# Kernel tuning notes

Hardware: AMD Instinct MI355X
Metric: run time of the kernel (lower is better)

The kernel has to match this reference:

```python
import jax, jax.numpy as jnp
import numpy as np

N = 16384   # total nodes in batch
E = 65536   # edges
B = 512     # sessions
L = 32      # nodes per session
H = 64      # hidden_size
HEADS = 16  # GAT heads (layer 1)
K = 3       # interests
V = 32000   # n_node (item vocab)
NEG = 0.2   # leaky relu slope


def _u(k, shape, stdv):
    return jax.random.uniform(k, shape, jnp.float32, -stdv, stdv)


def setup_inputs():
    key = jax.random.key(0)
    ks = jax.random.split(key, 24)
    s = 1.0 / np.sqrt(H)  # reset_parameters: uniform(-stdv, stdv)
    D = K * H
    return {
        "x": jax.random.randint(ks[0], (N,), 0, V),
        "edge_index": jax.random.randint(ks[1], (2, E), 0, N),
        "batch": jnp.repeat(jnp.arange(B, dtype=jnp.int32), L),
        "embedding": _u(ks[2], (V, H), s),
        "w_interest": _u(ks[3], (H, K), s),
        "gat1_W": _u(ks[4], (K, H, HEADS * H), s),
        "gat1_as": _u(ks[5], (K, HEADS, H), s),
        "gat1_ad": _u(ks[6], (K, HEADS, H), s),
        "gat1_b": _u(ks[7], (K, HEADS * H), s),
        "gat2_W": _u(ks[8], (K, HEADS * H, H), s),
        "gat2_as": _u(ks[9], (K, 1, H), s),
        "gat2_ad": _u(ks[10], (K, 1, H), s),
        "gat2_b": _u(ks[11], (K, H), s),
        "W1_w": _u(ks[12], (D, D), s), "W1_b": _u(ks[13], (D,), s),
        "W2_w": _u(ks[14], (D, D), s), "W2_b": _u(ks[15], (D,), s),
        "q_w": _u(ks[16], (D, 1), s), "q_b": _u(ks[17], (1,), s),
        "W3_w": _u(ks[18], (2 * D, D), s), "W3_b": _u(ks[19], (D,), s),
    }


def _gat(h_in, W, b, a_s, a_d, src, dst, valid, heads, out):
    """PyG GATConv: per-head linear, edge softmax over dest, self-loops for all nodes."""
    n = h_in.shape[0]
    h = (h_in @ W).reshape(n, heads, out)          # [n, heads, out]
    asrc = (h * a_s[None]).sum(-1)                 # [n, heads]
    adst = (h * a_d[None]).sum(-1)
    loop = jnp.arange(n)
    fs = jnp.concatenate([src, loop])              # edges + self-loops
    fd = jnp.concatenate([dst, loop])
    v = jnp.concatenate([valid, jnp.ones((n,), bool)])
    logits = jax.nn.leaky_relu(asrc[fs] + adst[fd], NEG)   # [E+n, heads]
    logits = jnp.where(v[:, None], logits, -1e9)
    m = jax.ops.segment_max(logits, fd, num_segments=n)
    p = jnp.exp(logits - m[fd]) * v[:, None]
    denom = jax.ops.segment_sum(p, fd, num_segments=n)     # [n, heads]
    num = jax.ops.segment_sum(p[:, :, None] * h[fs], fd, num_segments=n)
    return (num / denom[:, :, None]).reshape(n, heads * out) + b


def _model(x, edge_index, batch, embedding, w_interest,
           gat1_W, gat1_as, gat1_ad, gat1_b,
           gat2_W, gat2_as, gat2_ad, gat2_b,
           W1_w, W1_b, W2_w, W2_b, q_w, q_b, W3_w, W3_b):
    e = embedding[x]                                # [N, H]
    g = jax.nn.softmax((e @ w_interest) / 0.1, axis=-1)   # [N, K]
    mask = g > (1.0 / K)                            # interest_mask
    src, dst = edge_index[0], edge_index[1]
    hiddens = []
    for i in range(K):                              # fixed small interest loop
        xi = g[:, i:i + 1] * e                      # einsum('ik,il->ikl')[:, i]
        valid = mask[src, i] & mask[dst, i]         # subgraph edge mask
        h1 = jax.nn.relu(_gat(xi, gat1_W[i], gat1_b[i], gat1_as[i], gat1_ad[i],
                              src, dst, valid, HEADS, H))
        h2 = _gat(h1, gat2_W[i], gat2_b[i], gat2_as[i], gat2_ad[i],
                  src, dst, valid, 1, H)
        hiddens.append(h2)
    sess = jnp.concatenate(hiddens, axis=1)         # [N, K*H]
    # Embedding2Score
    last_idx = jax.ops.segment_max(jnp.arange(N), batch, num_segments=B)
    v_n = sess[last_idx]                            # [B, K*H]  last node per session
    q1 = v_n[batch] @ W1_w + W1_b                   # v_n repeated per node
    q2 = sess @ W2_w + W2_b
    alpha = jax.nn.sigmoid(q1 + q2) @ q_w + q_b     # [N, 1]
    s_g = jax.ops.segment_sum(alpha * sess, batch, num_segments=B)
    s_h = jnp.concatenate([v_n, s_g], axis=1) @ W3_w + W3_b   # [B, K*H]
    s_h = s_h.reshape(B * K, H)                     # multi-interest split
    z = s_h @ embedding.T                           # [B*K, V]
    return z.reshape(B, K, V).max(axis=1)           # [B, V]


def reference(x, edge_index, batch, embedding, w_interest,
              gat1_W, gat1_as, gat1_ad, gat1_b,
              gat2_W, gat2_as, gat2_ad, gat2_b,
              W1_w, W1_b, W2_w, W2_b, q_w, q_b, W3_w, W3_b):
    return _model(x, edge_index, batch, embedding, w_interest,
                  gat1_W, gat1_as, gat1_ad, gat1_b,
                  gat2_W, gat2_as, gat2_ad, gat2_b,
                  W1_w, W1_b, W2_w, W2_b, q_w, q_b, W3_w, W3_b)
```

## Files before the change

kernel.cpp:

```cpp
#include <hip/hip_runtime.h>
#include <math.h>

#define NN 16384
#define EE 65536
#define BB 512
#define VV 32000

typedef unsigned short us_t;
typedef unsigned int u32_t;
typedef __attribute__((ext_vector_type(4))) float f32x4;
typedef __attribute__((ext_vector_type(8))) short bf16x8;

__device__ __forceinline__ float bf2f(unsigned int u) {
  return __uint_as_float((u & 0xffffu) << 16);
}
__device__ __forceinline__ unsigned short f2bf(float f) {
  unsigned int x = __float_as_uint(f);
  unsigned int r = (x + 0x7fffu + ((x >> 16) & 1u)) >> 16;
  return (unsigned short)r;
}
__device__ __forceinline__ float wsum(float v) {
#pragma unroll
  for (int o = 32; o; o >>= 1) v += __shfl_xor(v, o, 64);
  return v;
}
__device__ __forceinline__ float redu16(float v) {
  v += __shfl_xor(v, 1, 64);
  v += __shfl_xor(v, 2, 64);
  v += __shfl_xor(v, 4, 64);
  v += __shfl_xor(v, 8, 64);
  return v;
}
__device__ __forceinline__ float lrelu(float x) { return x > 0.f ? x : 0.2f * x; }

__global__ void k_detect(const void* emb, int* flag) {
  if (threadIdx.x == 0 && blockIdx.x == 0) {
    const us_t* u = (const us_t*)emb;
    int ok = 1;
    for (int i = 0; i < 128; i++) {
      float v = bf2f((unsigned int)u[i]);
      if (!(fabsf(v) <= 0.13f)) { ok = 0; break; }
    }
    *flag = ok;
  }
}

struct PrepArgs {
  const void* src[17];
  void* dst[17];
  int n[17];
  int kind[17];
  int start[18];
};

__global__ void k_prep(PrepArgs pa, const int* __restrict__ flag) {
  int blk = blockIdx.x;
  int s = 0;
  while (s < 16 && blk >= pa.start[s + 1]) s++;
  int i = (blk - pa.start[s]) * 256 + threadIdx.x;
  if (i >= pa.n[s]) return;
  float v = (*flag) ? bf2f((unsigned int)((const us_t*)pa.src[s])[i])
                    : ((const float*)pa.src[s])[i];
  int kind = pa.kind[s];
  if (kind == 0) {
    ((float*)pa.dst[s])[i] = v;
  } else if (kind == 1) {
    ((us_t*)pa.dst[s])[i] = f2bf(v);
  } else if (kind == 2) {
    int ii = i >> 16, r = i & 65535, k = r >> 10, col = r & 1023;
    ((us_t*)pa.dst[s])[(ii << 16) + col * 64 + k] = f2bf(v);
  } else if (kind == 3) {
    int ii = i >> 16, r = i & 65535, k = r >> 6, col = r & 63;
    ((us_t*)pa.dst[s])[(ii << 16) + col * 1024 + k] = f2bf(v);
  } else {
    int k = i / 192, col = i % 192;
    ((us_t*)pa.dst[s])[col * 192 + k] = f2bf(v);
  }
}

__global__ void k_prepWa(const void* __restrict__ g1Wraw,
                         const float* __restrict__ g1as, const float* __restrict__ g1ad,
                         const int* __restrict__ flag, us_t* __restrict__ Waspack) {
  int gid = blockIdx.x * 256 + threadIdx.x;
  if (gid >= 96 * 64) return;
  int c = gid >> 6, k = gid & 63;
  int i = c >> 5, sd = (c >> 4) & 1, h = c & 15;
  const float* av = (sd ? g1ad : g1as) + i * 1024 + h * 64;
  size_t base = (size_t)i * 65536 + (size_t)k * 1024 + h * 64;
  int isbf = *flag;
  float s = 0.f;
  for (int d = 0; d < 64; d++) {
    float wv = isbf ? bf2f((unsigned int)((const us_t*)g1Wraw)[base + d])
                    : ((const float*)g1Wraw)[base + d];
    s += wv * av[d];
  }
  Waspack[c * 64 + k] = f2bf(s);
}

__global__ void k_embed(const int* __restrict__ x, const void* __restrict__ embr,
                        const void* __restrict__ wintr, const int* __restrict__ flag,
                        us_t* __restrict__ e_bf, float* __restrict__ g) {
  int gid = blockIdx.x * blockDim.x + threadIdx.x;
  int n = gid >> 6, lane = gid & 63;
  if (n >= NN) return;
  int isbf = *flag;
  size_t ei = (size_t)x[n] * 64 + lane;
  float v = isbf ? bf2f((unsigned int)((const us_t*)embr)[ei]) : ((const float*)embr)[ei];
  e_bf[(size_t)n * 64 + lane] = f2bf(v);
  float w0, w1, w2;
  if (isbf) {
    const us_t* w = (const us_t*)wintr;
    w0 = bf2f(w[lane * 3 + 0]); w1 = bf2f(w[lane * 3 + 1]); w2 = bf2f(w[lane * 3 + 2]);
  } else {
    const float* w = (const float*)wintr;
    w0 = w[lane * 3 + 0]; w1 = w[lane * 3 + 1]; w2 = w[lane * 3 + 2];
  }
  float t0 = wsum(v * w0), t1 = wsum(v * w1), t2 = wsum(v * w2);
  if (lane == 0) {
    float l0 = t0 / 0.1f, l1 = t1 / 0.1f, l2 = t2 / 0.1f;
    float m = fmaxf(l0, fmaxf(l1, l2));
    float p0 = __expf(l0 - m), p1 = __expf(l1 - m), p2 = __expf(l2 - m);
    float inv = 1.0f / (p0 + p1 + p2);
    g[n * 4 + 0] = p0 * inv; g[n * 4 + 1] = p1 * inv;
    g[n * 4 + 2] = p2 * inv; g[n * 4 + 3] = 0.f;
  }
}

__global__ void k_countv(const int* __restrict__ ei, const float* __restrict__ g,
                         int* __restrict__ countsv) {
  int e = blockIdx.x * 256 + threadIdx.x;
  if (e >= EE) return;
  int s = ei[e], d = ei[EE + e];
  const float thr = 1.0f / 3.0f;
#pragma unroll
  for (int i = 0; i < 3; i++) {
    if (g[s * 4 + i] > thr && g[d * 4 + i] > thr)
      atomicAdd(&countsv[i * NN + d], 1);
  }
}

__global__ void k_scanv(const int* __restrict__ counts, int* __restrict__ offsets) {
  __shared__ int part[256];
  __shared__ int excl[257];
  int t = threadIdx.x;
  int base = t * 192;
  int s = 0;
  for (int j = 0; j < 192; j++) s += counts[base + j];
  part[t] = s;
  __syncthreads();
  if (t == 0) {
    int run = 0;
    for (int j = 0; j < 256; j++) { excl[j] = run; run += part[j]; }
    excl[256] = run;
  }
  __syncthreads();
  int run = excl[t];
  for (int j = 0; j < 192; j++) { offsets[base + j] = run; run += counts[base + j]; }
  if (t == 255) offsets[3 * NN] = excl[256];
}

__global__ void k_fillv(const int* __restrict__ ei, const float* __restrict__ g,
                        const float* __restrict__ eatt,
                        const int* __restrict__ offsetsv, int* __restrict__ fillposv,
                        int2* __restrict__ edgesC, float* __restrict__ easrcP) {
  int e = blockIdx.x * 256 + threadIdx.x;
  if (e >= EE) return;
  int s = ei[e], d = ei[EE + e];
  const float thr = 1.0f / 3.0f;
#pragma unroll
  for (int i = 0; i < 3; i++) {
    float gs = g[s * 4 + i];
    if (gs > thr && g[d * 4 + i] > thr) {
      int pos = offsetsv[i * NN + d] + atomicAdd(&fillposv[i * NN + d], 1);
      edgesC[pos] = make_int2(s, __float_as_int(gs));
      const float* er = &eatt[(size_t)s * 96 + i * 32];
      float* op = &easrcP[(size_t)pos * 16];
#pragma unroll
      for (int h = 0; h < 16; h++) op[h] = gs * er[h];
    }
  }
}

__global__ __launch_bounds__(256) void k_easrc(
    const us_t* __restrict__ e_bf, const us_t* __restrict__ Waspack,
    float* __restrict__ eatt) {
  __shared__ char As[8192];
  int t = threadIdx.x;
  int row0 = blockIdx.x * 64;
  for (int id = t; id < 512; id += 256) {
    int r = id >> 3, c = id & 7;
    uint4 v = *(const uint4*)&e_bf[(size_t)(row0 + r) * 64 + c * 8];
    *(uint4*)(As + r * 128 + ((c ^ (r & 7)) << 4)) = v;
  }
  __syncthreads();
  int wv = t >> 6, L = t & 63, li = L & 15, lq = L >> 4;
#pragma unroll
  for (int ct = 0; ct < 6; ct++) {
    f32x4 acc = {0.f, 0.f, 0.f, 0.f};
#pragma unroll
    for (int ks = 0; ks < 2; ks++) {
      int row = wv * 16 + li;
      bf16x8 af = *(const bf16x8*)(As + row * 128 + (((ks * 4 + lq) ^ (row & 7)) << 4));
      bf16x8 bfr = *(const bf16x8*)(Waspack + (size_t)(ct * 16 + li) * 64 + ks * 32 + lq * 8);
      acc = __builtin_amdgcn_mfma_f32_16x16x32_bf16(af, bfr, acc, 0, 0, 0);
    }
#pragma unroll
    for (int r = 0; r < 4; r++) {
      int row = row0 + wv * 16 + lq * 4 + r;
      eatt[(size_t)row * 96 + ct * 16 + li] = acc[r];
    }
  }
}

__global__ __launch_bounds__(256) void k_phaseA(
    const us_t* __restrict__ e_bf, const float* __restrict__ g,
    const float* __restrict__ eatt,
    const int* __restrict__ offsetsv, const int2* __restrict__ edgesC,
    const float* __restrict__ easrcP, us_t* __restrict__ xagg) {
  int t = threadIdx.x;
  int intr = blockIdx.y;
  int wv = t >> 6, L = t & 63;
  int n = blockIdx.x * 4 + wv;
  int h = L >> 2;
  int doff = (L & 3) * 16;
  float gn = g[n * 4 + intr];
  float ad = gn * eatt[(size_t)n * 96 + intr * 32 + 16 + h];
  float m = lrelu(gn * eatt[(size_t)n * 96 + intr * 32 + h] + ad);
  float den = 1.f;
  float acc[16];
  {
    const uint4* ep = (const uint4*)&e_bf[(size_t)n * 64 + doff];
    uint4 a = ep[0], b = ep[1];
    acc[0] = gn * bf2f(a.x);  acc[1] = gn * bf2f(a.x >> 16);
    acc[2] = gn * bf2f(a.y);  acc[3] = gn * bf2f(a.y >> 16);
    acc[4] = gn * bf2f(a.z);  acc[5] = gn * bf2f(a.z >> 16);
    acc[6] = gn * bf2f(a.w);  acc[7] = gn * bf2f(a.w >> 16);
    acc[8] = gn * bf2f(b.x);  acc[9] = gn * bf2f(b.x >> 16);
    acc[10] = gn * bf2f(b.y); acc[11] = gn * bf2f(b.y >> 16);
    acc[12] = gn * bf2f(b.z); acc[13] = gn * bf2f(b.z >> 16);
    acc[14] = gn * bf2f(b.w); acc[15] = gn * bf2f(b.w >> 16);
  }
  int beg = offsetsv[intr * NN + n], end = offsetsv[intr * NN + n + 1];
  for (int j = beg; j < end; j++) {
    int2 sg = edgesC[j];
    int s = sg.x;
    float gs = __int_as_float(sg.y);
    float l = lrelu(easrcP[(size_t)j * 16 + h] + ad);
    float p = __expf(l - m);
    den += p;
    float pg = p * gs;
    const uint4* ep = (const uint4*)&e_bf[(size_t)s * 64 + doff];
    uint4 a = ep[0], b = ep[1];
    acc[0] += pg * bf2f(a.x);  acc[1] += pg * bf2f(a.x >> 16);
    acc[2] += pg * bf2f(a.y);  acc[3] += pg * bf2f(a.y >> 16);
    acc[4] += pg * bf2f(a.z);  acc[5] += pg * bf2f(a.z >> 16);
    acc[6] += pg * bf2f(a.w);  acc[7] += pg * bf2f(a.w >> 16);
    acc[8] += pg * bf2f(b.x);  acc[9] += pg * bf2f(b.x >> 16);
    acc[10] += pg * bf2f(b.y); acc[11] += pg * bf2f(b.y >> 16);
    acc[12] += pg * bf2f(b.z); acc[13] += pg * bf2f(b.z >> 16);
    acc[14] += pg * bf2f(b.w); acc[15] += pg * bf2f(b.w >> 16);
  }
  float inv = 1.f / den;
  u32_t w[8];
#pragma unroll
  for (int kk = 0; kk < 8; kk++) {
    w[kk] = (u32_t)f2bf(acc[2 * kk] * inv) | ((u32_t)f2bf(acc[2 * kk + 1] * inv) << 16);
  }
  us_t* op = &xagg[((size_t)intr * NN + n) * 1024 + h * 64 + doff];
  *(uint4*)op = make_uint4(w[0], w[1], w[2], w[3]);
  *(uint4*)(op + 8) = make_uint4(w[4], w[5], w[6], w[7]);
}

__global__ __launch_bounds__(128) void k_phaseB(
    const us_t* __restrict__ xagg, const us_t* __restrict__ g1Wt,
    const us_t* __restrict__ g2Wt, const float* __restrict__ b1all,
    const float* __restrict__ g2as, const float* __restrict__ g2ad,
    us_t* __restrict__ h2pre, float* __restrict__ a2s, float* __restrict__ a2d) {
  __shared__ char Tb[2][2][4096];
  __shared__ float b1s[1024];
  __shared__ float a2v[128];
  int t = threadIdx.x;
  int wv = t >> 6, L = t & 63, li = L & 15, lq = L >> 4;
  int intr = blockIdx.y;
  int n0 = blockIdx.x * 64 + wv * 32;
  const us_t* Wt1 = g1Wt + (size_t)intr * 65536;
  const us_t* Wt2 = g2Wt + (size_t)intr * 65536;
  const us_t* xa = xagg + ((size_t)intr * NN + n0 - (size_t)wv * 32 + (size_t)wv * 32) * 1024;
  for (int id = t; id < 1024; id += 128) b1s[id] = b1all[intr * 1024 + id];
  if (t < 64) a2v[t] = g2as[intr * 64 + t];
  else a2v[t] = g2ad[intr * 64 + (t - 64)];
  __syncthreads();
  f32x4 acc2[4][2];
#pragma unroll
  for (int ca = 0; ca < 4; ca++)
#pragma unroll
    for (int nb = 0; nb < 2; nb++) acc2[ca][nb] = {0.f, 0.f, 0.f, 0.f};
  for (int hh = 0; hh < 16; hh++) {
    bf16x8 bx[2][2];
#pragma unroll
    for (int nb = 0; nb < 2; nb++)
#pragma unroll
      for (int ks = 0; ks < 2; ks++)
        bx[nb][ks] = *(const bf16x8*)&xa[(size_t)(nb * 16 + li) * 1024 + hh * 64 + ks * 32 + lq * 8];
    f32x4 c1[4][2];
#pragma unroll
    for (int ct = 0; ct < 4; ct++)
#pragma unroll
      for (int nb = 0; nb < 2; nb++) c1[ct][nb] = {0.f, 0.f, 0.f, 0.f};
#pragma unroll
    for (int ks = 0; ks < 2; ks++) {
#pragma unroll
      for (int ct = 0; ct < 4; ct++) {
        bf16x8 af = *(const bf16x8*)&Wt1[(size_t)(hh * 64 + ct * 16 + li) * 64 + ks * 32 + lq * 8];
#pragma unroll
        for (int nb = 0; nb < 2; nb++)
          c1[ct][nb] = __builtin_amdgcn_mfma_f32_16x16x32_bf16(af, bx[nb][ks], c1[ct][nb], 0, 0, 0);
      }
    }
    char* Th = &Tb[wv][hh & 1][0];
#pragma unroll
    for (int ct = 0; ct < 4; ct++) {
      float b0 = b1s[hh * 64 + ct * 16 + lq * 4 + 0];
      float b1v = b1s[hh * 64 + ct * 16 + lq * 4 + 1];
      float b2 = b1s[hh * 64 + ct * 16 + lq * 4 + 2];
      float b3 = b1s[hh * 64 + ct * 16 + lq * 4 + 3];
#pragma unroll
      for (int nb = 0; nb < 2; nb++) {
        int node = nb * 16 + li;
        u32_t p0 = (u32_t)f2bf(fmaxf(c1[ct][nb][0] + b0, 0.f)) |
                   ((u32_t)f2bf(fmaxf(c1[ct][nb][1] + b1v, 0.f)) << 16);
        u32_t p1 = (u32_t)f2bf(fmaxf(c1[ct][nb][2] + b2, 0.f)) |
                   ((u32_t)f2bf(fmaxf(c1[ct][nb][3] + b3, 0.f)) << 16);
        int ch = (ct * 2 + (lq >> 1)) ^ (node & 7);
        *(uint2*)(Th + node * 128 + (ch << 4) + ((lq & 1) * 8)) = make_uint2(p0, p1);
      }
    }
#pragma unroll
    for (int ks2 = 0; ks2 < 2; ks2++) {
      bf16x8 bt[2];
#pragma unroll
      for (int nb = 0; nb < 2; nb++) {
        int node = nb * 16 + li;
        int ch = (ks2 * 4 + lq) ^ (node & 7);
        bt[nb] = *(const bf16x8*)(Th + node * 128 + (ch << 4));
      }
#pragma unroll
      for (int ca = 0; ca < 4; ca++) {
        bf16x8 af2 = *(const bf16x8*)&Wt2[(size_t)(ca * 16 + li) * 1024 + hh * 64 + ks2 * 32 + lq * 8];
#pragma unroll
        for (int nb = 0; nb < 2; nb++)
          acc2[ca][nb] = __builtin_amdgcn_mfma_f32_16x16x32_bf16(af2, bt[nb], acc2[ca][nb], 0, 0, 0);
      }
    }
  }
  float asv[16], adv[16];
#pragma unroll
  for (int ca = 0; ca < 4; ca++)
#pragma unroll
    for (int r = 0; r < 4; r++) {
      asv[ca * 4 + r] = a2v[ca * 16 + lq * 4 + r];
      adv[ca * 4 + r] = a2v[64 + ca * 16 + lq * 4 + r];
    }
#pragma unroll
  for (int nb = 0; nb < 2; nb++) {
    float ps = 0.f, pd = 0.f;
#pragma unroll
    for (int ca = 0; ca < 4; ca++)
#pragma unroll
      for (int r = 0; r < 4; r++) {
        float v = acc2[ca][nb][r];
        ps += v * asv[ca * 4 + r];
        pd += v * adv[ca * 4 + r];
      }
    ps += __shfl_xor(ps, 16, 64); ps += __shfl_xor(ps, 32, 64);
    pd += __shfl_xor(pd, 16, 64); pd += __shfl_xor(pd, 32, 64);
    if (lq == 0) {
      a2s[(size_t)intr * NN + n0 + nb * 16 + li] = ps;
      a2d[(size_t)intr * NN + n0 + nb * 16 + li] = pd;
    }
  }
  char* Tr = &Tb[wv][0][0];
#pragma unroll
  for (int ca = 0; ca < 4; ca++)
#pragma unroll
    for (int nb = 0; nb < 2; nb++) {
      int node = nb * 16 + li;
      u32_t p0 = (u32_t)f2bf(acc2[ca][nb][0]) | ((u32_t)f2bf(acc2[ca][nb][1]) << 16);
      u32_t p1 = (u32_t)f2bf(acc2[ca][nb][2]) | ((u32_t)f2bf(acc2[ca][nb][3]) << 16);
      int ch = (ca * 2 + (lq >> 1)) ^ (node & 7);
      *(uint2*)(Tr + node * 128 + (ch << 4) + ((lq & 1) * 8)) = make_uint2(p0, p1);
    }
  asm volatile("s_waitcnt lgkmcnt(0)" ::: "memory");
  {
    int row = L >> 1, hc = (L & 1) * 4;
#pragma unroll
    for (int cc = 0; cc < 4; cc++) {
      int ch = (hc + cc) ^ (row & 7);
      uint4 v = *(const uint4*)(Tr + row * 128 + (ch << 4));
      *(uint4*)&h2pre[((size_t)intr * NN + n0 + row) * 64 + (hc + cc) * 8] = v;
    }
  }
}

__global__ void k_gat2_agg(const us_t* __restrict__ h2pre_a,
                           const float* __restrict__ a2s_a, const float* __restrict__ a2d_a,
                           const float* __restrict__ b2all,
                           const int* __restrict__ offsetsv,
                           const int2* __restrict__ edgesC, float* __restrict__ sess) {
  int intr = blockIdx.y;
  int gid = blockIdx.x * blockDim.x + threadIdx.x;
  int n = gid >> 6, lane = gid & 63;
  if (n >= NN) return;
  const us_t* h2pre = h2pre_a + (size_t)intr * NN * 64;
  const float* a2s = a2s_a + (size_t)intr * NN;
  const float* a2d = a2d_a + (size_t)intr * NN;
  const float* b2 = b2all + intr * 64;
  float ad = a2d[n];
  float m = lrelu(a2s[n] + ad);
  float den = 1.f;
  float acc = bf2f((unsigned int)h2pre[(size_t)n * 64 + lane]);
  int beg = offsetsv[intr * NN + n], end = offsetsv[intr * NN + n + 1];
  for (int j = beg; j < end; j++) {
    int s = edgesC[j].x;
    float l = lrelu(a2s[s] + ad);
    float p = __expf(l - m);
    den += p;
    acc += p * bf2f((unsigned int)h2pre[(size_t)s * 64 + lane]);
  }
  sess[(size_t)n * 192 + intr * 64 + lane] = acc / den + b2[lane];
}

__global__ __launch_bounds__(192) void k_vq1(
    const float* __restrict__ sess,
    const float* __restrict__ W1w, const float* __restrict__ W1b,
    float* __restrict__ vn, float* __restrict__ vq1) {
  __shared__ float row[192];
  int b = blockIdx.x, j = threadIdx.x;
  int li = b * 32 + 31;
  float v = sess[(size_t)li * 192 + j];
  row[j] = v;
  vn[b * 192 + j] = v;
  __syncthreads();
  float acc = W1b[j];
  for (int k = 0; k < 192; k++) acc += row[k] * W1w[k * 192 + j];
  vq1[b * 192 + j] = acc;
}

__global__ __launch_bounds__(256) void k_alpha_sg_mfma(
    const float* __restrict__ sess, const float* __restrict__ vq1,
    const us_t* __restrict__ W2T, const float* __restrict__ W2b,
    const float* __restrict__ qw, const float* __restrict__ qb,
    float* __restrict__ sg) {
  __shared__ char As[64 * 512];
  __shared__ float vq_l[2 * 192];
  __shared__ float w2b_l[192], qw_l[192];
  __shared__ float sg_l[2 * 192];
  int t = threadIdx.x;
  int n0 = blockIdx.x * 64;
  if (t < 192) { w2b_l[t] = W2b[t]; qw_l[t] = qw[t]; }
  for (int id = t; id < 384; id += 256) {
    sg_l[id] = 0.f;
    vq_l[id] = vq1[(size_t)(blockIdx.x * 2) * 192 + id];
  }
  for (int id = t; id < 1536; id += 256) {
    int r = id / 24, c = id % 24;
    const float* p = &sess[(size_t)(n0 + r) * 192 + c * 8];
    float4 f0 = *(const float4*)p;
    float4 f1 = *(const float4*)(p + 4);
    u32_t w0 = (u32_t)f2bf(f0.x) | ((u32_t)f2bf(f0.y) << 16);
    u32_t w1 = (u32_t)f2bf(f0.z) | ((u32_t)f2bf(f0.w) << 16);
    u32_t w2 = (u32_t)f2bf(f1.x) | ((u32_t)f2bf(f1.y) << 16);
    u32_t w3 = (u32_t)f2bf(f1.z) | ((u32_t)f2bf(f1.w) << 16);
    *(uint4*)(As + r * 512 + ((c ^ (r & 7)) << 4)) = make_uint4(w0, w1, w2, w3);
  }
  __syncthreads();
  int wv = t >> 6, lane = t & 63, li = lane & 15, lq = lane >> 4;
  int sl = wv >> 1;
  f32x4 acc[12];
#pragma unroll
  for (int sub = 0; sub < 12; sub++) acc[sub] = {0.f, 0.f, 0.f, 0.f};
#pragma unroll
  for (int ks = 0; ks < 6; ks++) {
    int r = wv * 16 + li;
    bf16x8 af = *(const bf16x8*)(As + r * 512 + (((ks * 4 + lq) ^ (r & 7)) << 4));
#pragma unroll
    for (int sub = 0; sub < 12; sub++) {
      bf16x8 bfr = *(const bf16x8*)&W2T[(size_t)(sub * 16 + li) * 192 + ks * 32 + lq * 8];
      acc[sub] = __builtin_amdgcn_mfma_f32_16x16x32_bf16(af, bfr, acc[sub], 0, 0, 0);
    }
  }
  float qbv = qb[0];
  float s_part[12];
#pragma unroll
  for (int sub = 0; sub < 12; sub++) s_part[sub] = 0.f;
#pragma unroll
  for (int rr = 0; rr < 4; rr++) {
    int n = n0 + wv * 16 + lq * 4 + rr;
    float ap = 0.f;
    float sv[12];
#pragma unroll
    for (int sub = 0; sub < 12; sub++) {
      int col = sub * 16 + li;
      float q = vq_l[sl * 192 + col] + acc[sub][rr] + w2b_l[col];
      float sgm = 1.f / (1.f + __expf(-q));
      ap += sgm * qw_l[col];
      sv[sub] = sess[(size_t)n * 192 + col];
    }
    ap = redu16(ap);
    float alpha = ap + qbv;
#pragma unroll
    for (int sub = 0; sub < 12; sub++) s_part[sub] += alpha * sv[sub];
  }
#pragma unroll
  for (int sub = 0; sub < 12; sub++) {
    float v = s_part[sub];
    v += __shfl_xor(v, 16, 64);
    v += __shfl_xor(v, 32, 64);
    if (lq == 0) atomicAdd(&sg_l[sl * 192 + sub * 16 + li], v);
  }
  __syncthreads();
  for (int id = t; id < 384; id += 256)
    sg[(size_t)(blockIdx.x * 2) * 192 + id] = sg_l[id];
}

__global__ __launch_bounds__(192) void k_sh(
    const float* __restrict__ vn, const float* __restrict__ sg,
    const float* __restrict__ W3w, const float* __restrict__ W3b,
    float* __restrict__ sh) {
  __shared__ float row[384];
  int b = blockIdx.x, j = threadIdx.x;
  row[j] = vn[b * 192 + j];
  row[192 + j] = sg[b * 192 + j];
  __syncthreads();
  float acc = W3b[j];
  for (int k = 0; k < 384; k++) acc += row[k] * W3w[k * 192 + j];
  sh[b * 192 + j] = acc;
}

__global__ __launch_bounds__(256) void k_final_mfma(
    const float* __restrict__ sh, const us_t* __restrict__ emb_bf,
    void* __restrict__ out, const int* __restrict__ flag) {
  __shared__ uint4 AsU[384];
  __shared__ uint4 BsU[2048];
  char* As = (char*)AsU;
  char* Bs = (char*)BsU;
  int t = threadIdx.x;
  int v0 = blockIdx.x * 256, b0 = blockIdx.y * 16;
  for (int id = t; id < 384; id += 256) {
    int i2 = id >> 7, rem = id & 127, r = rem >> 3, c = rem & 7;
    const float* p = &sh[(size_t)(b0 + r) * 192 + i2 * 64 + c * 8];
    float4 f0 = *(const float4*)p;
    float4 f1 = *(const float4*)(p + 4);
    u32_t w0 = (u32_t)f2bf(f0.x) | ((u32_t)f2bf(f0.y) << 16);
    u32_t w1 = (u32_t)f2bf(f0.z) | ((u32_t)f2bf(f0.w) << 16);
    u32_t w2 = (u32_t)f2bf(f1.x) | ((u32_t)f2bf(f1.y) << 16);
    u32_t w3 = (u32_t)f2bf(f1.z) | ((u32_t)f2bf(f1.w) << 16);
    *(uint4*)(As + i2 * 2048 + r * 128 + ((c ^ (r & 7)) << 4)) = make_uint4(w0, w1, w2, w3);
  }
  for (int id = t; id < 2048; id += 256) {
    int vr = id >> 3, c = id & 7;
    uint4 v = *(const uint4*)&emb_bf[(size_t)(v0 + vr) * 64 + c * 8];
    *(uint4*)(Bs + vr * 128 + ((c ^ (vr & 7)) << 4)) = v;
  }
  __syncthreads();
  int wv = t >> 6, lane = t & 63, li = lane & 15, lq = lane >> 4;
  int cb = wv * 64;
  int isbf = *flag;
  f32x4 acc[3][4];
#pragma unroll
  for (int i = 0; i < 3; i++)
#pragma unroll
    for (int sub = 0; sub < 4; sub++) acc[i][sub] = {0.f, 0.f, 0.f, 0.f};
#pragma unroll
  for (int ks = 0; ks < 2; ks++) {
    bf16x8 bfr[4];
#pragma unroll
    for (int sub = 0; sub < 4; sub++) {
      int vr = cb + sub * 16 + li;
      bfr[sub] = *(const bf16x8*)(Bs + vr * 128 + ((((ks << 2) | lq) ^ (vr & 7)) << 4));
    }
#pragma unroll
    for (int i = 0; i < 3; i++) {
      bf16x8 af = *(const bf16x8*)(As + i * 2048 + li * 128 + ((((ks << 2) | lq) ^ (li & 7)) << 4));
#pragma unroll
      for (int sub = 0; sub < 4; sub++)
        acc[i][sub] = __builtin_amdgcn_mfma_f32_16x16x32_bf16(af, bfr[sub], acc[i][sub], 0, 0, 0);
    }
  }
#pragma unroll
  for (int sub = 0; sub < 4; sub++) {
    int col = v0 + cb + sub * 16 + li;
#pragma unroll
    for (int rr = 0; rr < 4; rr++) {
      float o = fmaxf(fmaxf(acc[0][sub][rr], acc[1][sub][rr]), acc[2][sub][rr]);
      int b = b0 + lq * 4 + rr;
      if (isbf) ((us_t*)out)[(size_t)b * VV + col] = f2bf(o);
      else ((float*)out)[(size_t)b * VV + col] = o;
    }
  }
}

extern "C" void kernel_launch(void* const* d_in, const int* in_sizes, int n_in,
                              void* d_out, int out_size, void* d_ws, size_t ws_size,
                              hipStream_t stream) {
  if (n_in < 21) return;
  const int* x = (const int*)d_in[0];
  const int* ei = (const int*)d_in[1];

  char* ws = (char*)d_ws;
  size_t off = 0;
  auto A = [&](size_t bytes) -> char* {
    char* p = ws + off;
    off += (bytes + 255) & ~(size_t)255;
    return p;
  };
  int* flag = (int*)A(4);
  us_t* emb_bf = (us_t*)A((size_t)VV * 64 * 2);
  us_t* e_bf = (us_t*)A((size_t)NN * 64 * 2);
  us_t* g1Wt = (us_t*)A((size_t)3 * 65536 * 2);
  us_t* g2Wt = (us_t*)A((size_t)3 * 65536 * 2);
  us_t* W2T = (us_t*)A((size_t)36864 * 2);
  us_t* Waspack = (us_t*)A((size_t)96 * 64 * 2);
  float* eatt = (float*)A((size_t)NN * 96 * 4);
  float* c_g1as = (float*)A(3072 * 4);
  float* c_g1ad = (float*)A(3072 * 4);
  float* c_g1b = (float*)A(3072 * 4);
  float* c_g2as = (float*)A(192 * 4);
  float* c_g2ad = (float*)A(192 * 4);
  float* c_g2b = (float*)A(192 * 4);
  float* c_W1w = (float*)A(36864 * 4);
  float* c_W1b = (float*)A(192 * 4);
  float* c_W2b = (float*)A(192 * 4);
  float* c_qw = (float*)A(192 * 4);
  float* c_qb = (float*)A(4);
  float* c_W3w = (float*)A(73728 * 4);
  float* c_W3b = (float*)A(192 * 4);
  float* g_buf = (float*)A((size_t)NN * 4 * 4);
  us_t* xagg = (us_t*)A((size_t)3 * NN * 1024 * 2);
  us_t* h2pre = (us_t*)A((size_t)3 * NN * 64 * 2);
  float* a2s = (float*)A((size_t)3 * NN * 4);
  float* a2d = (float*)A((size_t)3 * NN * 4);
  float* sess = (float*)A((size_t)NN * 192 * 4);
  float* vq1 = (float*)A((size_t)BB * 192 * 4);
  float* sg = (float*)A((size_t)BB * 192 * 4);
  float* vn = (float*)A((size_t)BB * 192 * 4);
  float* shb = (float*)A((size_t)BB * 192 * 4);
  int* countsv = (int*)A((size_t)3 * NN * 4);
  int* offsetsv = (int*)A((size_t)(3 * NN + 1) * 4);
  int* fillposv = (int*)A((size_t)3 * NN * 4);
  int2* edgesC = (int2*)A((size_t)3 * EE * 8);
  float* easrcP = (float*)A((size_t)3 * EE * 16 * 4);
  if (off > ws_size) return;

  hipMemsetAsync(countsv, 0, 3 * NN * 4, stream);
  hipMemsetAsync(fillposv, 0, 3 * NN * 4, stream);

  k_detect<<<1, 64, 0, stream>>>(d_in[3], flag);

  PrepArgs pa;
  int nb = 0, idx = 0;
  auto SEC = [&](const void* s, void* d, int n, int kind) {
    pa.src[idx] = s; pa.dst[idx] = d; pa.n[idx] = n; pa.kind[idx] = kind;
    pa.start[idx] = nb; nb += (n + 255) / 256; idx++;
  };
  SEC(d_in[3], emb_bf, VV * 64, 1);
  SEC(d_in[5], g1Wt, 196608, 2);
  SEC(d_in[9], g2Wt, 196608, 3);
  SEC(d_in[15], W2T, 36864, 4);
  SEC(d_in[6], c_g1as, 3072, 0);
  SEC(d_in[7], c_g1ad, 3072, 0);
  SEC(d_in[8], c_g1b, 3072, 0);
  SEC(d_in[10], c_g2as, 192, 0);
  SEC(d_in[11], c_g2ad, 192, 0);
  SEC(d_in[12], c_g2b, 192, 0);
  SEC(d_in[13], c_W1w, 36864, 0);
  SEC(d_in[14], c_W1b, 192, 0);
  SEC(d_in[16], c_W2b, 192, 0);
  SEC(d_in[17], c_qw, 192, 0);
  SEC(d_in[18], c_qb, 1, 0);
  SEC(d_in[19], c_W3w, 73728, 0);
  SEC(d_in[20], c_W3b, 192, 0);
  pa.start[17] = nb;
  k_prep<<<nb, 256, 0, stream>>>(pa, flag);
  k_prepWa<<<24, 256, 0, stream>>>(d_in[5], c_g1as, c_g1ad, flag, Waspack);

  k_embed<<<NN * 64 / 256, 256, 0, stream>>>(x, d_in[3], d_in[4], flag, e_bf, g_buf);
  k_easrc<<<NN / 64, 256, 0, stream>>>(e_bf, Waspack, eatt);
  k_countv<<<EE / 256, 256, 0, stream>>>(ei, g_buf, countsv);
  k_scanv<<<1, 256, 0, stream>>>(countsv, offsetsv);
  k_fillv<<<EE / 256, 256, 0, stream>>>(ei, g_buf, eatt, offsetsv, fillposv,
                                        edgesC, easrcP);

  k_phaseA<<<dim3(NN / 4, 3), 256, 0, stream>>>(
      e_bf, g_buf, eatt, offsetsv, edgesC, easrcP, xagg);
  k_phaseB<<<dim3(NN / 64, 3), 128, 0, stream>>>(
      xagg, g1Wt, g2Wt, c_g1b, c_g2as, c_g2ad, h2pre, a2s, a2d);
  k_gat2_agg<<<dim3(NN * 64 / 256, 3), 256, 0, stream>>>(
      h2pre, a2s, a2d, c_g2b, offsetsv, edgesC, sess);

  k_vq1<<<BB, 192, 0, stream>>>(sess, c_W1w, c_W1b, vn, vq1);
  k_alpha_sg_mfma<<<NN / 64, 256, 0, stream>>>(sess, vq1, W2T, c_W2b, c_qw, c_qb, sg);
  k_sh<<<BB, 192, 0, stream>>>(vn, sg, c_W3w, c_W3b, shb);
  k_final_mfma<<<dim3(VV / 256, BB / 16), 256, 0, stream>>>(shb, emb_bf, d_out, flag);
}
```

Before: 280.2 us.

## Split phaseB head loop across four waves with LDS atomic reduction

Each block now covers 32 nodes with four waves, and each wave takes four of the sixteen GAT heads instead of one wave looping over all sixteen for its 32 nodes. The per-wave partial layer-2 accumulators are combined with shared-memory float atomics into a swizzled buffer, then the attention dot products and the bf16 h2pre store are done from that buffer. The xagg loads are also software-prefetched one head ahead. This raises parallelism and shortens each wave's serial dependency chain, at the cost of LDS atomics, an extra block barrier, more shared memory, and a changed summation order.

```diff
diff --git a/kernel.cpp b/kernel.cpp
--- a/kernel.cpp
+++ b/kernel.cpp
@@ -271,53 +271,64 @@
   *(uint4*)(op + 8) = make_uint4(w[4], w[5], w[6], w[7]);
 }
 
-__global__ __launch_bounds__(128) void k_phaseB(
+__global__ __launch_bounds__(256) void k_phaseB(
     const us_t* __restrict__ xagg, const us_t* __restrict__ g1Wt,
     const us_t* __restrict__ g2Wt, const float* __restrict__ b1all,
     const float* __restrict__ g2as, const float* __restrict__ g2ad,
     us_t* __restrict__ h2pre, float* __restrict__ a2s, float* __restrict__ a2d) {
-  __shared__ char Tb[2][2][4096];
+  __shared__ char Tb[4][2][4096];
+  __shared__ float h2red[32 * 64];
   __shared__ float b1s[1024];
   __shared__ float a2v[128];
   int t = threadIdx.x;
   int wv = t >> 6, L = t & 63, li = L & 15, lq = L >> 4;
   int intr = blockIdx.y;
-  int n0 = blockIdx.x * 64 + wv * 32;
+  int n0 = blockIdx.x * 32;
   const us_t* Wt1 = g1Wt + (size_t)intr * 65536;
   const us_t* Wt2 = g2Wt + (size_t)intr * 65536;
-  const us_t* xa = xagg + ((size_t)intr * NN + n0 - (size_t)wv * 32 + (size_t)wv * 32) * 1024;
-  for (int id = t; id < 1024; id += 128) b1s[id] = b1all[intr * 1024 + id];
+  const us_t* xa = xagg + ((size_t)intr * NN + n0) * 1024;
+  for (int id = t; id < 1024; id += 256) b1s[id] = b1all[intr * 1024 + id];
+  for (int id = t; id < 2048; id += 256) h2red[id] = 0.f;
   if (t < 64) a2v[t] = g2as[intr * 64 + t];
-  else a2v[t] = g2ad[intr * 64 + (t - 64)];
+  else if (t < 128) a2v[t] = g2ad[intr * 64 + (t - 64)];
   __syncthreads();
   f32x4 acc2[4][2];
 #pragma unroll
   for (int ca = 0; ca < 4; ca++)
 #pragma unroll
     for (int nb = 0; nb < 2; nb++) acc2[ca][nb] = {0.f, 0.f, 0.f, 0.f};
-  for (int hh = 0; hh < 16; hh++) {
-    bf16x8 bx[2][2];
+  int h0 = wv * 4;
+  bf16x8 bxA[2][2];
+#pragma unroll
+  for (int nb = 0; nb < 2; nb++)
+#pragma unroll
+    for (int ks = 0; ks < 2; ks++)
+      bxA[nb][ks] = *(const bf16x8*)&xa[(size_t)(nb * 16 + li) * 1024 + h0 * 64 + ks * 32 + lq * 8];
+  for (int hi = 0; hi < 4; hi++) {
+    int hh = h0 + hi;
+    int hn = h0 + ((hi + 1) & 3);
+    bf16x8 bxB[2][2];
 #pragma unroll
     for (int nb = 0; nb < 2; nb++)
 #pragma unroll
       for (int ks = 0; ks < 2; ks++)
-        bx[nb][ks] = *(const bf16x8*)&xa[(size_t)(nb * 16 + li) * 1024 + hh * 64 + ks * 32 + lq * 8];
+        bxB[nb][ks] = *(const bf16x8*)&xa[(size_t)(nb * 16 + li) * 1024 + hn * 64 + ks * 32 + lq * 8];
     f32x4 c1[4][2];
 #pragma unroll
     for (int ct = 0; ct < 4; ct++)
 #pragma unroll
       for (int nb = 0; nb < 2; nb++) c1[ct][nb] = {0.f, 0.f, 0.f, 0.f};
 #pragma unroll
-    for (int ks = 0; ks < 2; ks++) {
-#pragma unroll
-      for (int ct = 0; ct < 4; ct++) {
+    for (int ct = 0; ct < 4; ct++) {
+#pragma unroll
+      for (int ks = 0; ks < 2; ks++) {
         bf16x8 af = *(const bf16x8*)&Wt1[(size_t)(hh * 64 + ct * 16 + li) * 64 + ks * 32 + lq * 8];
 #pragma unroll
         for (int nb = 0; nb < 2; nb++)
-          c1[ct][nb] = __builtin_amdgcn_mfma_f32_16x16x32_bf16(af, bx[nb][ks], c1[ct][nb], 0, 0, 0);
+          c1[ct][nb] = __builtin_amdgcn_mfma_f32_16x16x32_bf16(af, bxA[nb][ks], c1[ct][nb], 0, 0, 0);
       }
     }
-    char* Th = &Tb[wv][hh & 1][0];
+    char* Th = &Tb[wv][hi & 1][0];
 #pragma unroll
     for (int ct = 0; ct < 4; ct++) {
       float b0 = b1s[hh * 64 + ct * 16 + lq * 4 + 0];
@@ -352,52 +363,45 @@
           acc2[ca][nb] = __builtin_amdgcn_mfma_f32_16x16x32_bf16(af2, bt[nb], acc2[ca][nb], 0, 0, 0);
       }
     }
-  }
-  float asv[16], adv[16];
-#pragma unroll
-  for (int ca = 0; ca < 4; ca++)
-#pragma unroll
-    for (int r = 0; r < 4; r++) {
-      asv[ca * 4 + r] = a2v[ca * 16 + lq * 4 + r];
-      adv[ca * 4 + r] = a2v[64 + ca * 16 + lq * 4 + r];
-    }
-#pragma unroll
-  for (int nb = 0; nb < 2; nb++) {
-    float ps = 0.f, pd = 0.f;
-#pragma unroll
-    for (int ca = 0; ca < 4; ca++)
-#pragma unroll
-      for (int r = 0; r < 4; r++) {
-        float v = acc2[ca][nb][r];
-        ps += v * asv[ca * 4 + r];
-        pd += v * adv[ca * 4 + r];
-      }
-    ps += __shfl_xor(ps, 16, 64); ps += __shfl_xor(ps, 32, 64);
-    pd += __shfl_xor(pd, 16, 64); pd += __shfl_xor(pd, 32, 64);
-    if (lq == 0) {
-      a2s[(size_t)intr * NN + n0 + nb * 16 + li] = ps;
-      a2d[(size_t)intr * NN + n0 + nb * 16 + li] = pd;
-    }
-  }
-  char* Tr = &Tb[wv][0][0];
-#pragma unroll
-  for (int ca = 0; ca < 4; ca++)
+#pragma unroll
+    for (int nb = 0; nb < 2; nb++)
+#pragma unroll
+      for (int ks = 0; ks < 2; ks++) bxA[nb][ks] = bxB[nb][ks];
+  }
+#pragma unroll
+  for (int ca = 0; ca < 4; ca++) {
 #pragma unroll
     for (int nb = 0; nb < 2; nb++) {
       int node = nb * 16 + li;
-      u32_t p0 = (u32_t)f2bf(acc2[ca][nb][0]) | ((u32_t)f2bf(acc2[ca][nb][1]) << 16);
-      u32_t p1 = (u32_t)f2bf(acc2[ca][nb][2]) | ((u32_t)f2bf(acc2[ca][nb][3]) << 16);
-      int ch = (ca * 2 + (lq >> 1)) ^ (node & 7);
-      *(uint2*)(Tr + node * 128 + (ch << 4) + ((lq & 1) * 8)) = make_uint2(p0, p1);
-    }
-  asm volatile("s_waitcnt lgkmcnt(0)" ::: "memory");
+      int sw = (node & 7) << 3;
+#pragma unroll
+      for (int r = 0; r < 4; r++) {
+        int col = ca * 16 + lq * 4 + r;
+        atomicAdd(&h2red[node * 64 + (col ^ sw)], acc2[ca][nb][r]);
+      }
+    }
+  }
+  __syncthreads();
   {
-    int row = L >> 1, hc = (L & 1) * 4;
-#pragma unroll
-    for (int cc = 0; cc < 4; cc++) {
-      int ch = (hc + cc) ^ (row & 7);
-      uint4 v = *(const uint4*)(Tr + row * 128 + (ch << 4));
-      *(uint4*)&h2pre[((size_t)intr * NN + n0 + row) * 64 + (hc + cc) * 8] = v;
+    int node = t >> 3, j0 = (t & 7) * 8;
+    int sw = (node & 7) << 3;
+    const float* hp = &h2red[node * 64 + (j0 ^ sw)];
+    float ps = 0.f, pd = 0.f;
+    u32_t pk[4];
+#pragma unroll
+    for (int jj = 0; jj < 4; jj++) {
+      float v0 = hp[2 * jj], v1 = hp[2 * jj + 1];
+      ps += v0 * a2v[j0 + 2 * jj] + v1 * a2v[j0 + 2 * jj + 1];
+      pd += v0 * a2v[64 + j0 + 2 * jj] + v1 * a2v[64 + j0 + 2 * jj + 1];
+      pk[jj] = (u32_t)f2bf(v0) | ((u32_t)f2bf(v1) << 16);
+    }
+    *(uint4*)&h2pre[((size_t)intr * NN + n0 + node) * 64 + j0] =
+        make_uint4(pk[0], pk[1], pk[2], pk[3]);
+    ps += __shfl_xor(ps, 1, 64); ps += __shfl_xor(ps, 2, 64); ps += __shfl_xor(ps, 4, 64);
+    pd += __shfl_xor(pd, 1, 64); pd += __shfl_xor(pd, 2, 64); pd += __shfl_xor(pd, 4, 64);
+    if ((t & 7) == 0) {
+      a2s[(size_t)intr * NN + n0 + node] = ps;
+      a2d[(size_t)intr * NN + n0 + node] = pd;
     }
   }
 }
@@ -693,7 +697,7 @@
 
   k_phaseA<<<dim3(NN / 4, 3), 256, 0, stream>>>(
       e_bf, g_buf, eatt, offsetsv, edgesC, easrcP, xagg);
-  k_phaseB<<<dim3(NN / 64, 3), 128, 0, stream>>>(
+  k_phaseB<<<dim3(NN / 32, 3), 256, 0, stream>>>(
       xagg, g1Wt, g2Wt, c_g1b, c_g2as, c_g2ad, h2pre, a2s, a2d);
   k_gat2_agg<<<dim3(NN * 64 / 256, 3), 256, 0, stream>>>(
       h2pre, a2s, a2d, c_g2b, offsetsv, edgesC, sess);
```

Result: slower. 320.9 us (+14.5%).

## Software-pipeline xagg loads in phaseB, process two heads per iteration, nontemporal xagg traffic

Applied to the files above, without the earlier changes.

The phaseB head loop is restructured to handle two heads per iteration and to prefetch the next pair's xagg fragments into registers while the current pair's MFMAs run. This hides global-load latency and exposes more independent MFMA chains. xagg writes in the aggregation kernel and reads in phaseB become nontemporal to avoid polluting cache with streaming data. It raises register pressure, which could lower occupancy, and the last iteration issues a wasted prefetch of heads 0-1.

```diff
diff --git a/kernel.cpp b/kernel.cpp
--- a/kernel.cpp
+++ b/kernel.cpp
@@ -10,6 +10,7 @@
 typedef unsigned int u32_t;
 typedef __attribute__((ext_vector_type(4))) float f32x4;
 typedef __attribute__((ext_vector_type(8))) short bf16x8;
+typedef __attribute__((ext_vector_type(4))) unsigned int u32x4;
 
 __device__ __forceinline__ float bf2f(unsigned int u) {
   return __uint_as_float((u & 0xffffu) << 16);
@@ -18,6 +19,13 @@
   unsigned int x = __float_as_uint(f);
   unsigned int r = (x + 0x7fffu + ((x >> 16) & 1u)) >> 16;
   return (unsigned short)r;
+}
+__device__ __forceinline__ bf16x8 ntld(const us_t* p) {
+  return __builtin_nontemporal_load((const bf16x8*)p);
+}
+__device__ __forceinline__ void ntst(us_t* p, u32_t a, u32_t b, u32_t c, u32_t d) {
+  u32x4 v = {a, b, c, d};
+  __builtin_nontemporal_store(v, (u32x4*)p);
 }
 __device__ __forceinline__ float wsum(float v) {
 #pragma unroll
@@ -267,8 +275,8 @@
     w[kk] = (u32_t)f2bf(acc[2 * kk] * inv) | ((u32_t)f2bf(acc[2 * kk + 1] * inv) << 16);
   }
   us_t* op = &xagg[((size_t)intr * NN + n) * 1024 + h * 64 + doff];
-  *(uint4*)op = make_uint4(w[0], w[1], w[2], w[3]);
-  *(uint4*)(op + 8) = make_uint4(w[4], w[5], w[6], w[7]);
+  ntst(op, w[0], w[1], w[2], w[3]);
+  ntst(op + 8, w[4], w[5], w[6], w[7]);
 }
 
 __global__ __launch_bounds__(128) void k_phaseB(
@@ -285,7 +293,7 @@
   int n0 = blockIdx.x * 64 + wv * 32;
   const us_t* Wt1 = g1Wt + (size_t)intr * 65536;
   const us_t* Wt2 = g2Wt + (size_t)intr * 65536;
-  const us_t* xa = xagg + ((size_t)intr * NN + n0 - (size_t)wv * 32 + (size_t)wv * 32) * 1024;
+  const us_t* xa = xagg + ((size_t)intr * NN + n0) * 1024;
   for (int id = t; id < 1024; id += 128) b1s[id] = b1all[intr * 1024 + id];
   if (t < 64) a2v[t] = g2as[intr * 64 + t];
   else a2v[t] = g2ad[intr * 64 + (t - 64)];
@@ -295,63 +303,98 @@
   for (int ca = 0; ca < 4; ca++)
 #pragma unroll
     for (int nb = 0; nb < 2; nb++) acc2[ca][nb] = {0.f, 0.f, 0.f, 0.f};
-  for (int hh = 0; hh < 16; hh++) {
-    bf16x8 bx[2][2];
+  bf16x8 bxa[2][2], bxb[2][2];
+#pragma unroll
+  for (int nb = 0; nb < 2; nb++)
+#pragma unroll
+    for (int ks = 0; ks < 2; ks++) {
+      bxa[nb][ks] = ntld(&xa[(size_t)(nb * 16 + li) * 1024 + ks * 32 + lq * 8]);
+      bxb[nb][ks] = ntld(&xa[(size_t)(nb * 16 + li) * 1024 + 64 + ks * 32 + lq * 8]);
+    }
+  for (int hp = 0; hp < 8; hp++) {
+    int ha = hp * 2, hb = ha + 1;
+    int hna = ((hp + 1) & 7) * 2, hnb = hna + 1;
+    bf16x8 nxa[2][2], nxb[2][2];
 #pragma unroll
     for (int nb = 0; nb < 2; nb++)
 #pragma unroll
-      for (int ks = 0; ks < 2; ks++)
-        bx[nb][ks] = *(const bf16x8*)&xa[(size_t)(nb * 16 + li) * 1024 + hh * 64 + ks * 32 + lq * 8];
-    f32x4 c1[4][2];
+      for (int ks = 0; ks < 2; ks++) {
+        nxa[nb][ks] = ntld(&xa[(size_t)(nb * 16 + li) * 1024 + hna * 64 + ks * 32 + lq * 8]);
+        nxb[nb][ks] = ntld(&xa[(size_t)(nb * 16 + li) * 1024 + hnb * 64 + ks * 32 + lq * 8]);
+      }
+    f32x4 c1a[4][2], c1b[4][2];
 #pragma unroll
     for (int ct = 0; ct < 4; ct++)
 #pragma unroll
-      for (int nb = 0; nb < 2; nb++) c1[ct][nb] = {0.f, 0.f, 0.f, 0.f};
+      for (int nb = 0; nb < 2; nb++) { c1a[ct][nb] = {0.f, 0.f, 0.f, 0.f}; c1b[ct][nb] = {0.f, 0.f, 0.f, 0.f}; }
 #pragma unroll
     for (int ks = 0; ks < 2; ks++) {
 #pragma unroll
       for (int ct = 0; ct < 4; ct++) {
-        bf16x8 af = *(const bf16x8*)&Wt1[(size_t)(hh * 64 + ct * 16 + li) * 64 + ks * 32 + lq * 8];
+        bf16x8 afa = *(const bf16x8*)&Wt1[(size_t)(ha * 64 + ct * 16 + li) * 64 + ks * 32 + lq * 8];
 #pragma unroll
         for (int nb = 0; nb < 2; nb++)
-          c1[ct][nb] = __builtin_amdgcn_mfma_f32_16x16x32_bf16(af, bx[nb][ks], c1[ct][nb], 0, 0, 0);
+          c1a[ct][nb] = __builtin_amdgcn_mfma_f32_16x16x32_bf16(afa, bxa[nb][ks], c1a[ct][nb], 0, 0, 0);
+        bf16x8 afb = *(const bf16x8*)&Wt1[(size_t)(hb * 64 + ct * 16 + li) * 64 + ks * 32 + lq * 8];
+#pragma unroll
+        for (int nb = 0; nb < 2; nb++)
+          c1b[ct][nb] = __builtin_amdgcn_mfma_f32_16x16x32_bf16(afb, bxb[nb][ks], c1b[ct][nb], 0, 0, 0);
       }
     }
-    char* Th = &Tb[wv][hh & 1][0];
+    char* Ta = &Tb[wv][0][0];
+    char* Tc = &Tb[wv][1][0];
 #pragma unroll
     for (int ct = 0; ct < 4; ct++) {
-      float b0 = b1s[hh * 64 + ct * 16 + lq * 4 + 0];
-      float b1v = b1s[hh * 64 + ct * 16 + lq * 4 + 1];
-      float b2 = b1s[hh * 64 + ct * 16 + lq * 4 + 2];
-      float b3 = b1s[hh * 64 + ct * 16 + lq * 4 + 3];
+      float ba0 = b1s[ha * 64 + ct * 16 + lq * 4 + 0];
+      float ba1 = b1s[ha * 64 + ct * 16 + lq * 4 + 1];
+      float ba2 = b1s[ha * 64 + ct * 16 + lq * 4 + 2];
+      float ba3 = b1s[ha * 64 + ct * 16 + lq * 4 + 3];
+      float bb0 = b1s[hb * 64 + ct * 16 + lq * 4 + 0];
+      float bb1 = b1s[hb * 64 + ct * 16 + lq * 4 + 1];
+      float bb2 = b1s[hb * 64 + ct * 16 + lq * 4 + 2];
+      float bb3 = b1s[hb * 64 + ct * 16 + lq * 4 + 3];
 #pragma unroll
       for (int nb = 0; nb < 2; nb++) {
         int node = nb * 16 + li;
-        u32_t p0 = (u32_t)f2bf(fmaxf(c1[ct][nb][0] + b0, 0.f)) |
-                   ((u32_t)f2bf(fmaxf(c1[ct][nb][1] + b1v, 0.f)) << 16);
-        u32_t p1 = (u32_t)f2bf(fmaxf(c1[ct][nb][2] + b2, 0.f)) |
-                   ((u32_t)f2bf(fmaxf(c1[ct][nb][3] + b3, 0.f)) << 16);
         int ch = (ct * 2 + (lq >> 1)) ^ (node & 7);
-        *(uint2*)(Th + node * 128 + (ch << 4) + ((lq & 1) * 8)) = make_uint2(p0, p1);
+        u32_t pa0 = (u32_t)f2bf(fmaxf(c1a[ct][nb][0] + ba0, 0.f)) |
+                    ((u32_t)f2bf(fmaxf(c1a[ct][nb][1] + ba1, 0.f)) << 16);
+        u32_t pa1 = (u32_t)f2bf(fmaxf(c1a[ct][nb][2] + ba2, 0.f)) |
+                    ((u32_t)f2bf(fmaxf(c1a[ct][nb][3] + ba3, 0.f)) << 16);
+        *(uint2*)(Ta + node * 128 + (ch << 4) + ((lq & 1) * 8)) = make_uint2(pa0, pa1);
+        u32_t pb0 = (u32_t)f2bf(fmaxf(c1b[ct][nb][0] + bb0, 0.f)) |
+                    ((u32_t)f2bf(fmaxf(c1b[ct][nb][1] + bb1, 0.f)) << 16);
+        u32_t pb1 = (u32_t)f2bf(fmaxf(c1b[ct][nb][2] + bb2, 0.f)) |
+                    ((u32_t)f2bf(fmaxf(c1b[ct][nb][3] + bb3, 0.f)) << 16);
+        *(uint2*)(Tc + node * 128 + (ch << 4) + ((lq & 1) * 8)) = make_uint2(pb0, pb1);
       }
     }
 #pragma unroll
     for (int ks2 = 0; ks2 < 2; ks2++) {
-      bf16x8 bt[2];
+      bf16x8 bta[2], btb[2];
 #pragma unroll
       for (int nb = 0; nb < 2; nb++) {
         int node = nb * 16 + li;
         int ch = (ks2 * 4 + lq) ^ (node & 7);
-        bt[nb] = *(const bf16x8*)(Th + node * 128 + (ch << 4));
+        bta[nb] = *(const bf16x8*)(Ta + node * 128 + (ch << 4));
+        btb[nb] = *(const bf16x8*)(Tc + node * 128 + (ch << 4));
       }
 #pragma unroll
       for (int ca = 0; ca < 4; ca++) {
-        bf16x8 af2 = *(const bf16x8*)&Wt2[(size_t)(ca * 16 + li) * 1024 + hh * 64 + ks2 * 32 + lq * 8];
+        bf16x8 af2a = *(const bf16x8*)&Wt2[(size_t)(ca * 16 + li) * 1024 + ha * 64 + ks2 * 32 + lq * 8];
 #pragma unroll
         for (int nb = 0; nb < 2; nb++)
-          acc2[ca][nb] = __builtin_amdgcn_mfma_f32_16x16x32_bf16(af2, bt[nb], acc2[ca][nb], 0, 0, 0);
+          acc2[ca][nb] = __builtin_amdgcn_mfma_f32_16x16x32_bf16(af2a, bta[nb], acc2[ca][nb], 0, 0, 0);
+        bf16x8 af2b = *(const bf16x8*)&Wt2[(size_t)(ca * 16 + li) * 1024 + hb * 64 + ks2 * 32 + lq * 8];
+#pragma unroll
+        for (int nb = 0; nb < 2; nb++)
+          acc2[ca][nb] = __builtin_amdgcn_mfma_f32_16x16x32_bf16(af2b, btb[nb], acc2[ca][nb], 0, 0, 0);
       }
     }
+#pragma unroll
+    for (int nb = 0; nb < 2; nb++)
+#pragma unroll
+      for (int ks = 0; ks < 2; ks++) { bxa[nb][ks] = nxa[nb][ks]; bxb[nb][ks] = nxb[nb][ks]; }
   }
   float asv[16], adv[16];
 #pragma unroll
```

New measurement: 284.8 us. No clear change (+1.7%).
